# Kernel tuning notes

Hardware: AMD Instinct MI355X
Metric: run time of the kernel (lower is better)

## Reference

```python
import jax, jax.numpy as jnp
import numpy as np

N_HEAD = 12

def setup_inputs() -> dict:
    key = jax.random.key(0)
    ks = jax.random.split(key, 5)
    B, T, C = 4, 2048, 768
    x = jax.random.normal(ks[0], (B, T, C), dtype=jnp.float32)
    s_in = 1.0 / np.sqrt(C)
    W_qkv = jax.random.normal(ks[1], (C, 3 * C), dtype=jnp.float32) * s_in
    b_qkv = jnp.zeros((3 * C,), dtype=jnp.float32)
    W_proj = jax.random.normal(ks[2], (C, C), dtype=jnp.float32) * s_in
    b_proj = jnp.zeros((C,), dtype=jnp.float32)
    return {"x": x, "W_qkv": W_qkv, "b_qkv": b_qkv, "W_proj": W_proj, "b_proj": b_proj}


def reference(x, W_qkv, b_qkv, W_proj, b_proj):
    B, T, C = x.shape
    H = N_HEAD
    D = C // H  # head dim
    qkv = x @ W_qkv + b_qkv                      # [B,T,3C]
    q, k, v = jnp.split(qkv, 3, axis=-1)
    # [B,T,C] -> [B,H,T,D]
    q = q.reshape(B, T, H, D).transpose(0, 2, 1, 3)
    k = k.reshape(B, T, H, D).transpose(0, 2, 1, 3)
    v = v.reshape(B, T, H, D).transpose(0, 2, 1, 3)
    att = jnp.einsum("bhqd,bhkd->bhqk", q, k) / jnp.sqrt(jnp.asarray(D, x.dtype))
    causal = jnp.tril(jnp.ones((T, T), dtype=bool))
    att = jnp.where(causal, att, jnp.asarray(-jnp.inf, att.dtype))
    att = jax.nn.softmax(att, axis=-1)
    y = jnp.einsum("bhqk,bhkd->bhqd", att, v)    # [B,H,T,D]
    y = y.transpose(0, 2, 1, 3).reshape(B, T, C)
    return y @ W_proj + b_proj
```

## Files before the change

### kernel.cpp

```cpp
#include <hip/hip_runtime.h>
#include <hip/hip_bf16.h>

typedef __bf16 bf16x8 __attribute__((ext_vector_type(8)));
typedef float f32x4 __attribute__((ext_vector_type(4)));
typedef unsigned int u32x4 __attribute__((ext_vector_type(4)));
typedef unsigned int u32x2 __attribute__((ext_vector_type(2)));
typedef int i32x2 __attribute__((ext_vector_type(2)));
typedef unsigned short u16;
typedef unsigned long long u64;

#define WAITVM(n) asm volatile("s_waitcnt vmcnt(" #n ")" ::: "memory")
#define SBAR() asm volatile("s_barrier" ::: "memory")

__device__ __forceinline__ u16 f2bf(float f) {
  unsigned u = __builtin_bit_cast(unsigned, f);
  u += 0x7FFFu + ((u >> 16) & 1u);
  return (u16)(u >> 16);
}
__device__ __forceinline__ unsigned cvtpk(float a, float b) {
  float2 f; f.x = a; f.y = b;
  __hip_bfloat162 h = __float22bfloat162_rn(f);
  unsigned u;
  __builtin_memcpy(&u, &h, 4);
  return u;
}

__device__ __forceinline__ void plswap(unsigned &a, unsigned &b) {
  i32x2 r = __builtin_amdgcn_permlane32_swap((int)a, (int)b, false, false);
  a = (unsigned)r[0];
  b = (unsigned)r[1];
}

__device__ __forceinline__ void gll16(const u16* g, u16* l) {
  __builtin_amdgcn_global_load_lds(
      (const __attribute__((address_space(1))) unsigned int*)g,
      (__attribute__((address_space(3))) unsigned int*)l, 16, 0, 0);
}

__global__ void cast_x_kernel(const float* __restrict__ in, u16* __restrict__ out, int n4) {
  int i = blockIdx.x * blockDim.x + threadIdx.x;
  if (i >= n4) return;
  f32x4 v = *(const f32x4*)(in + (size_t)i * 4);
  u32x2 pk;
  pk[0] = cvtpk(v[0], v[1]);
  pk[1] = cvtpk(v[2], v[3]);
  *(u32x2*)(out + (size_t)i * 4) = pk;
}

__global__ void transpose_cast_kernel(const float* __restrict__ W, u16* __restrict__ WT, int K, int N) {
  __shared__ float tile[32][33];
  int c0 = blockIdx.x * 32, r0 = blockIdx.y * 32;
  int tx = threadIdx.x & 31, tg = threadIdx.x >> 5;
#pragma unroll
  for (int i = 0; i < 4; ++i) {
    int r = tg + i * 8;
    tile[r][tx] = W[(size_t)(r0 + r) * N + c0 + tx];
  }
  __syncthreads();
#pragma unroll
  for (int i = 0; i < 4; ++i) {
    int r = tg + i * 8;
    WT[(size_t)(c0 + r) * K + r0 + tx] = f2bf(tile[tx][r]);
  }
}

__global__ __launch_bounds__(256, 4) void gemm_qkv_kernel(
    const u16* __restrict__ A, const u16* __restrict__ BT, const float* __restrict__ bias,
    u16* __restrict__ Qb, u16* __restrict__ Kb, u16* __restrict__ Vt) {
  constexpr int K = 768;
  constexpr int NS = K / 32;
  __shared__ u16 Asm[2][128 * 32];
  __shared__ u16 Bsm[2][128 * 32];
  const int lin = blockIdx.y * 18 + blockIdx.x;
  const int swz = (lin & 7) * 144 + (lin >> 3);
  const int bxn = swz % 18, byn = swz / 18;
  const int tid = threadIdx.x;
  const int w = tid >> 6, lane = tid & 63;
  const int l15 = lane & 15, quad = lane >> 4;
  const int srow = tid >> 2, scol = (tid & 3) * 8;
  const int m0 = byn * 128, n0 = bxn * 128;
  const u16* Ag = A + (size_t)(m0 + srow) * K + scol;
  const u16* Bg = BT + (size_t)(n0 + srow) * K + scol;
  const int mw = (w >> 1) * 64, nw = (w & 1) * 64;
  f32x4 acc[4][4];
#pragma unroll
  for (int i = 0; i < 4; ++i)
#pragma unroll
    for (int j = 0; j < 4; ++j) acc[i][j] = {0.f, 0.f, 0.f, 0.f};

  auto STAGE = [&](int buf, int ks) {
    const u16* a = Ag + ks * 32;
    const u16* b = Bg + ks * 32;
#pragma unroll
    for (int rb = 0; rb < 2; ++rb) {
      gll16(a + (size_t)rb * 64 * K, &Asm[buf][(rb * 64 + w * 16) * 32]);
      gll16(b + (size_t)rb * 64 * K, &Bsm[buf][(rb * 64 + w * 16) * 32]);
    }
  };
  auto COMPUTE = [&](int buf) {
    bf16x8 af[4], bfj[4];
#pragma unroll
    for (int i = 0; i < 4; ++i) af[i] = *(const bf16x8*)&Asm[buf][(mw + i * 16 + l15) * 32 + quad * 8];
#pragma unroll
    for (int j = 0; j < 4; ++j) bfj[j] = *(const bf16x8*)&Bsm[buf][(nw + j * 16 + l15) * 32 + quad * 8];
#pragma unroll
    for (int i = 0; i < 4; ++i)
#pragma unroll
      for (int j = 0; j < 4; ++j)
        acc[i][j] = __builtin_amdgcn_mfma_f32_16x16x32_bf16(af[i], bfj[j], acc[i][j], 0, 0, 0);
  };

  STAGE(0, 0);
  for (int s = 0; s + 2 < NS; s += 2) {
    STAGE(1, s + 1); WAITVM(4); SBAR(); COMPUTE(0); SBAR();
    STAGE(0, s + 2); WAITVM(4); SBAR(); COMPUTE(1); SBAR();
  }
  STAGE(1, NS - 1); WAITVM(4); SBAR(); COMPUTE(0);
  WAITVM(0); SBAR(); COMPUTE(1);

  const int sec = bxn / 6;
  const int nbase = n0 - sec * 768;
#pragma unroll
  for (int j = 0; j < 4; ++j) {
    const int nloc = nbase + nw + j * 16 + l15;
    const float bv = bias[sec * 768 + nloc];
    const int h = nloc >> 6, d = nloc & 63;
#pragma unroll
    for (int i = 0; i < 4; ++i) {
      const int m = m0 + mw + i * 16 + quad * 4;
      const int bb = m >> 11, trow = m & 2047;
      if (sec == 2) {
        u32x2 pk;
        pk[0] = cvtpk(acc[i][j][0] + bv, acc[i][j][1] + bv);
        pk[1] = cvtpk(acc[i][j][2] + bv, acc[i][j][3] + bv);
        *(u32x2*)(Vt + (size_t)((bb * 12 + h) * 64 + d) * 2048 + trow) = pk;
      } else {
        u16* dst = (sec == 0) ? Qb : Kb;
        const float scl = (sec == 0) ? 0.125f * 1.44269504f : 1.0f;
#pragma unroll
        for (int r = 0; r < 4; ++r)
          dst[(size_t)((bb * 12 + h) * 2048 + trow + r) * 64 + d] = f2bf((acc[i][j][r] + bv) * scl);
      }
    }
  }
}

__global__ __launch_bounds__(256, 4) void gemm_proj_kernel(
    const u16* __restrict__ A, const u16* __restrict__ BT, const float* __restrict__ bias,
    float* __restrict__ out) {
  constexpr int K = 768;
  constexpr int NS = K / 32;
  __shared__ u16 Asm[2][64 * 32];
  __shared__ u16 Bsm[2][128 * 32];
  const int lin = blockIdx.y * 6 + blockIdx.x;
  const int swz = (lin & 7) * 96 + (lin >> 3);
  const int tid = threadIdx.x;
  const int w = tid >> 6, lane = tid & 63;
  const int l15 = lane & 15, quad = lane >> 4;
  const int srow = tid >> 2, scol = (tid & 3) * 8;
  const int m0 = (swz / 6) * 64, n0 = (swz % 6) * 128;
  const u16* Ag = A + (size_t)(m0 + srow) * K + scol;
  const u16* Bg = BT + (size_t)(n0 + srow) * K + scol;
  const int mw = (w >> 1) * 32, nw = (w & 1) * 64;
  f32x4 acc[2][4];
#pragma unroll
  for (int i = 0; i < 2; ++i)
#pragma unroll
    for (int j = 0; j < 4; ++j) acc[i][j] = {0.f, 0.f, 0.f, 0.f};

  auto STAGE = [&](int buf, int ks) {
    const u16* a = Ag + ks * 32;
    const u16* b = Bg + ks * 32;
    gll16(a, &Asm[buf][(w * 16) * 32]);
#pragma unroll
    for (int rb = 0; rb < 2; ++rb)
      gll16(b + (size_t)rb * 64 * K, &Bsm[buf][(rb * 64 + w * 16) * 32]);
  };
  auto COMPUTE = [&](int buf) {
    bf16x8 af[2], bfj[4];
#pragma unroll
    for (int i = 0; i < 2; ++i) af[i] = *(const bf16x8*)&Asm[buf][(mw + i * 16 + l15) * 32 + quad * 8];
#pragma unroll
    for (int j = 0; j < 4; ++j) bfj[j] = *(const bf16x8*)&Bsm[buf][(nw + j * 16 + l15) * 32 + quad * 8];
#pragma unroll
    for (int i = 0; i < 2; ++i)
#pragma unroll
      for (int j = 0; j < 4; ++j)
        acc[i][j] = __builtin_amdgcn_mfma_f32_16x16x32_bf16(af[i], bfj[j], acc[i][j], 0, 0, 0);
  };

  STAGE(0, 0);
  for (int s = 0; s + 2 < NS; s += 2) {
    STAGE(1, s + 1); WAITVM(3); SBAR(); COMPUTE(0); SBAR();
    STAGE(0, s + 2); WAITVM(3); SBAR(); COMPUTE(1); SBAR();
  }
  STAGE(1, NS - 1); WAITVM(3); SBAR(); COMPUTE(0);
  WAITVM(0); SBAR(); COMPUTE(1);

#pragma unroll
  for (int j = 0; j < 4; ++j) {
    const int n = n0 + nw + j * 16 + l15;
    const float bv = bias[n];
#pragma unroll
    for (int i = 0; i < 2; ++i) {
      const int m = m0 + mw + i * 16 + quad * 4;
#pragma unroll
      for (int r = 0; r < 4; ++r) out[(size_t)(m + r) * 768 + n] = acc[i][j][r] + bv;
    }
  }
}

__global__ __launch_bounds__(512) void attn_split_kernel(
    const u16* __restrict__ Qg, const u16* __restrict__ Kg, const u16* __restrict__ Vtg,
    u16* __restrict__ Yb, float* __restrict__ Opart, float* __restrict__ lpart) {
  constexpr int T = 2048, D = 64;
  constexpr int LDP = 72;
  constexpr float MBOUND = 20.0f;
  __shared__ u16 Ks[2][64 * LDP];
  __shared__ u16 VTs[2][64 * LDP];
  const int lin = blockIdx.y * 40 + blockIdx.x;
  const int swzb = (lin & 7) * 240 + (lin >> 3);
  const int s = 39 - (swzb % 40);
  const int bh = swzb / 40;
  int qt2, c;
  if (s < 4) { qt2 = s; c = 0; }
  else if (s < 12) { qt2 = 4 + ((s - 4) >> 1); c = (s - 4) & 1; }
  else if (s < 24) { int u = s - 12; int q3 = u / 3; qt2 = 8 + q3; c = u - 3 * q3; }
  else { int u = s - 24; qt2 = 12 + (u >> 2); c = u & 3; }
  const int nkt = 2 * qt2 + 2;
  const int niter = min(8, nkt - 8 * c);
  const int tid = threadIdx.x;
  const int w = tid >> 6, lane = tid & 63;
  const int l15 = lane & 15, quad = lane >> 4;
  const int srow = tid >> 3;
  const int scol = (tid & 7) * 8;
  const int so0 = scol - 4 * (tid & 1);
  const int so1 = scol + 8 - 4 * (tid & 1);
  const u16* Kp = Kg + (size_t)bh * T * D;
  const u16* VTp = Vtg + (size_t)bh * D * T;

  const int wdiag = 2 * qt2 + (w >> 2);
  const int qq = qt2 * 128 + w * 16 + l15;
  const u16* qrow = Qg + ((size_t)bh * T + qq) * D;
  const bf16x8 qfa = *(const bf16x8*)(qrow + quad * 8);
  const bf16x8 qfb = *(const bf16x8*)(qrow + 32 + quad * 8);

  u32x4 onesw; onesw[0] = 0x3F803F80u; onesw[1] = 0x3F803F80u; onesw[2] = 0x3F803F80u; onesw[3] = 0x3F803F80u;
  const bf16x8 ones = __builtin_bit_cast(bf16x8, onesw);

  f32x4 o[4] = {{0,0,0,0},{0,0,0,0},{0,0,0,0},{0,0,0,0}};
  f32x4 lacc = {0.f, 0.f, 0.f, 0.f};

  u32x4 kA, vA;
  auto LOADT = [&](int kt) {
    const int k1 = kt * 64;
    kA = *(const u32x4*)(Kp + (size_t)(k1 + srow) * D + scol);
    vA = *(const u32x4*)(VTp + (size_t)srow * T + k1 + scol);
  };
  auto STORET = [&](int buf) {
    *(u32x4*)&Ks[buf][srow * LDP + scol] = kA;
    u32x2 vlo; vlo[0] = vA[0]; vlo[1] = vA[1];
    u32x2 vhi; vhi[0] = vA[2]; vhi[1] = vA[3];
    *(u32x2*)&VTs[buf][srow * LDP + so0] = vlo;
    *(u32x2*)&VTs[buf][srow * LDP + so1] = vhi;
  };

  LOADT(c * 8);
  STORET(0);
  if (niter > 1) LOADT(c * 8 + 1);
  __syncthreads();

  for (int j = 0; j < niter; ++j) {
    const int buf = j & 1;
    const int ktg = c * 8 + j;
    if (ktg <= wdiag) {
      f32x4 sA[4];
#pragma unroll
      for (int t = 0; t < 4; ++t) sA[t] = {-MBOUND, -MBOUND, -MBOUND, -MBOUND};
      __builtin_amdgcn_s_setprio(1);
#pragma unroll
      for (int t = 0; t < 4; ++t) {
        const bf16x8 kf0 = *(const bf16x8*)&Ks[buf][(t * 16 + l15) * LDP + quad * 8];
        const bf16x8 kf1 = *(const bf16x8*)&Ks[buf][(t * 16 + l15) * LDP + 32 + quad * 8];
        sA[t] = __builtin_amdgcn_mfma_f32_16x16x32_bf16(kf0, qfa, sA[t], 0, 0, 0);
        sA[t] = __builtin_amdgcn_mfma_f32_16x16x32_bf16(kf1, qfb, sA[t], 0, 0, 0);
      }
      __builtin_amdgcn_s_setprio(0);
      if (ktg == wdiag) {
        const int k0 = ktg * 64;
#pragma unroll
        for (int t = 0; t < 4; ++t)
#pragma unroll
          for (int r = 0; r < 4; ++r)
            if (k0 + t * 16 + quad * 4 + r > qq) sA[t][r] = -1e30f;
      }
      unsigned W[4][2];
#pragma unroll
      for (int t = 0; t < 4; ++t) {
        float e0 = __builtin_amdgcn_exp2f(sA[t][0]);
        float e1 = __builtin_amdgcn_exp2f(sA[t][1]);
        float e2 = __builtin_amdgcn_exp2f(sA[t][2]);
        float e3 = __builtin_amdgcn_exp2f(sA[t][3]);
        W[t][0] = cvtpk(e0, e1);
        W[t][1] = cvtpk(e2, e3);
      }
      plswap(W[0][0], W[1][0]);
      plswap(W[0][1], W[1][1]);
      plswap(W[2][0], W[3][0]);
      plswap(W[2][1], W[3][1]);
      u32x4 paw; paw[0] = W[0][0]; paw[1] = W[0][1]; paw[2] = W[1][0]; paw[3] = W[1][1];
      u32x4 pbw; pbw[0] = W[2][0]; pbw[1] = W[2][1]; pbw[2] = W[3][0]; pbw[3] = W[3][1];
      const bf16x8 pa = __builtin_bit_cast(bf16x8, paw);
      const bf16x8 pb = __builtin_bit_cast(bf16x8, pbw);
      __builtin_amdgcn_s_setprio(1);
      lacc = __builtin_amdgcn_mfma_f32_16x16x32_bf16(ones, pa, lacc, 0, 0, 0);
      lacc = __builtin_amdgcn_mfma_f32_16x16x32_bf16(ones, pb, lacc, 0, 0, 0);
#pragma unroll
      for (int t = 0; t < 4; ++t) {
        const bf16x8 vf0 = *(const bf16x8*)&VTs[buf][(t * 16 + l15) * LDP + quad * 8];
        const bf16x8 vf1 = *(const bf16x8*)&VTs[buf][(t * 16 + l15) * LDP + 32 + quad * 8];
        o[t] = __builtin_amdgcn_mfma_f32_16x16x32_bf16(vf0, pa, o[t], 0, 0, 0);
        o[t] = __builtin_amdgcn_mfma_f32_16x16x32_bf16(vf1, pb, o[t], 0, 0, 0);
      }
      __builtin_amdgcn_s_setprio(0);
    }
    if (j + 1 < niter) {
      STORET(buf ^ 1);
      if (j + 2 < niter) LOADT(c * 8 + j + 2);
    }
    __syncthreads();
  }

  const float lv = lacc[0];
  if (qt2 <= 3) {
    const float inv = 1.f / lv;
    const int bidx = bh / 12, hidx = bh % 12;
    u16* y = Yb + ((size_t)bidx * T + qq) * 768 + hidx * 64;
#pragma unroll
    for (int t = 0; t < 4; ++t) {
      u32x2 pk;
      pk[0] = cvtpk(o[t][0] * inv, o[t][1] * inv);
      pk[1] = cvtpk(o[t][2] * inv, o[t][3] * inv);
      *(u32x2*)(y + t * 16 + quad * 4) = pk;
    }
  } else {
    const size_t pidx = (size_t)bh * 40 + s;
    float* Op = Opart + pidx * 8192 + (size_t)(w * 16 + l15) * 64;
#pragma unroll
    for (int t = 0; t < 4; ++t) *(f32x4*)(Op + t * 16 + quad * 4) = o[t];
    if (quad == 0) lpart[pidx * 128 + w * 16 + l15] = lv;
  }
}

__global__ __launch_bounds__(256) void attn_combine_kernel(
    const float* __restrict__ Opart, const float* __restrict__ lpart, u16* __restrict__ Yb) {
  constexpr int T = 2048;
  const int qt2 = 4 + blockIdx.x;
  const int bh = blockIdx.y;
  const int nch = (qt2 < 8) ? 2 : (qt2 < 12) ? 3 : 4;
  const int off = (qt2 < 8) ? 4 + (qt2 - 4) * 2 : (qt2 < 12) ? 12 + (qt2 - 8) * 3 : 24 + (qt2 - 12) * 4;
  const size_t base = (size_t)bh * 40 + off;
  const int tid = threadIdx.x;
  const int q = tid >> 1, db = (tid & 1) * 32;
  f32x4 o[8] = {{0,0,0,0},{0,0,0,0},{0,0,0,0},{0,0,0,0},{0,0,0,0},{0,0,0,0},{0,0,0,0},{0,0,0,0}};
  float l = 0.f;
  for (int cc = 0; cc < nch; ++cc) {
    const float* Op = Opart + (base + cc) * 8192 + (size_t)q * 64 + db;
#pragma unroll
    for (int v = 0; v < 8; ++v) o[v] += *(const f32x4*)(Op + v * 4);
    l += lpart[(base + cc) * 128 + q];
  }
  const float inv = 1.f / l;
  const int bidx = bh / 12, hidx = bh % 12;
  u16* y = Yb + ((size_t)bidx * T + qt2 * 128 + q) * 768 + hidx * 64 + db;
#pragma unroll
  for (int g = 0; g < 2; ++g) {
    u32x4 pk;
    pk[0] = cvtpk(o[g * 4 + 0][0] * inv, o[g * 4 + 0][1] * inv);
    pk[1] = cvtpk(o[g * 4 + 0][2] * inv, o[g * 4 + 0][3] * inv);
    pk[2] = cvtpk(o[g * 4 + 1][0] * inv, o[g * 4 + 1][1] * inv);
    pk[3] = cvtpk(o[g * 4 + 1][2] * inv, o[g * 4 + 1][3] * inv);
    *(u32x4*)(y + g * 16) = pk;
    pk[0] = cvtpk(o[g * 4 + 2][0] * inv, o[g * 4 + 2][1] * inv);
    pk[1] = cvtpk(o[g * 4 + 2][2] * inv, o[g * 4 + 2][3] * inv);
    pk[2] = cvtpk(o[g * 4 + 3][0] * inv, o[g * 4 + 3][1] * inv);
    pk[3] = cvtpk(o[g * 4 + 3][2] * inv, o[g * 4 + 3][3] * inv);
    *(u32x4*)(y + g * 16 + 8) = pk;
  }
}

__global__ __launch_bounds__(256) void attn_kernel(
    const u16* __restrict__ Qg, const u16* __restrict__ Kg, const u16* __restrict__ Vtg,
    u16* __restrict__ Yb) {
  constexpr int T = 2048, D = 64;
  constexpr int LDP = 72;
  constexpr float MBOUND = 20.0f;
  __shared__ u16 Ks[64 * LDP];
  __shared__ u16 VTs[64 * LDP];
  __shared__ u16 Ps[4 * 32 * LDP];
  const int qb = 15 - blockIdx.x;
  const int bh = blockIdx.y;
  const int Q0 = qb * 128;
  const int bidx = bh / 12, hidx = bh % 12;
  const int tid = threadIdx.x;
  const int w = tid >> 6, lane = tid & 63;
  const int l15 = lane & 15, quad = lane >> 4;
  const int srow = tid >> 2, scol = (tid & 3) * 16;
  const u16* Kp = Kg + (size_t)bh * T * D;
  const u16* VTp = Vtg + (size_t)bh * D * T;
  u16* pw0 = &Ps[(w * 32) * LDP];
  u16* pw1 = &Ps[(w * 32 + 16) * LDP];
  const u16* qrow0 = Qg + ((size_t)bh * T + Q0 + w * 16 + l15) * D;
  const bf16x8 qf0a = *(const bf16x8*)(qrow0 + quad * 8);
  const bf16x8 qf0b = *(const bf16x8*)(qrow0 + 32 + quad * 8);
  const bf16x8 qf1a = *(const bf16x8*)(qrow0 + (size_t)64 * D + quad * 8);
  const bf16x8 qf1b = *(const bf16x8*)(qrow0 + (size_t)64 * D + 32 + quad * 8);
  const int qq0 = Q0 + w * 16 + l15, qq1 = qq0 + 64;
  f32x4 o0[4] = {{0,0,0,0},{0,0,0,0},{0,0,0,0},{0,0,0,0}};
  f32x4 o1[4] = {{0,0,0,0},{0,0,0,0},{0,0,0,0},{0,0,0,0}};
  float l0v = 0.f, l1v = 0.f;
  const int nkt = 2 * qb + 2;
  u32x4 kA = *(const u32x4*)(Kp + (size_t)srow * D + scol);
  u32x4 kB = *(const u32x4*)(Kp + (size_t)srow * D + scol + 8);
  u32x4 vA = *(const u32x4*)(VTp + (size_t)srow * T + scol);
  u32x4 vB = *(const u32x4*)(VTp + (size_t)srow * T + scol + 8);
  for (int kt = 0; kt < nkt; ++kt) {
    __syncthreads();
    *(u32x4*)&Ks[srow * LDP + scol] = kA;
    *(u32x4*)&Ks[srow * LDP + scol + 8] = kB;
    *(u32x4*)&VTs[srow * LDP + scol] = vA;
    *(u32x4*)&VTs[srow * LDP + scol + 8] = vB;
    __syncthreads();
    if (kt + 1 < nkt) {
      const int k1 = (kt + 1) * 64;
      kA = *(const u32x4*)(Kp + (size_t)(k1 + srow) * D + scol);
      kB = *(const u32x4*)(Kp + (size_t)(k1 + srow) * D + scol + 8);
      vA = *(const u32x4*)(VTp + (size_t)srow * T + k1 + scol);
      vB = *(const u32x4*)(VTp + (size_t)srow * T + k1 + scol + 8);
    }
    const int k0 = kt * 64;
    const bool g0a = (kt <= 2 * qb);
    f32x4 s0[4] = {{0,0,0,0},{0,0,0,0},{0,0,0,0},{0,0,0,0}};
    f32x4 s1[4] = {{0,0,0,0},{0,0,0,0},{0,0,0,0},{0,0,0,0}};
#pragma unroll
    for (int t = 0; t < 4; ++t) {
      const bf16x8 kf0 = *(const bf16x8*)&Ks[(t * 16 + l15) * LDP + quad * 8];
      const bf16x8 kf1 = *(const bf16x8*)&Ks[(t * 16 + l15) * LDP + 32 + quad * 8];
      s0[t] = __builtin_amdgcn_mfma_f32_16x16x32_bf16(kf0, qf0a, s0[t], 0, 0, 0);
      s0[t] = __builtin_amdgcn_mfma_f32_16x16x32_bf16(kf1, qf0b, s0[t], 0, 0, 0);
      s1[t] = __builtin_amdgcn_mfma_f32_16x16x32_bf16(kf0, qf1a, s1[t], 0, 0, 0);
      s1[t] = __builtin_amdgcn_mfma_f32_16x16x32_bf16(kf1, qf1b, s1[t], 0, 0, 0);
    }
    if (g0a) {
      if (kt == 2 * qb) {
#pragma unroll
        for (int t = 0; t < 4; ++t)
#pragma unroll
          for (int r = 0; r < 4; ++r)
            if (k0 + t * 16 + quad * 4 + r > qq0) s0[t][r] = -1e30f;
      }
#pragma unroll
      for (int t = 0; t < 4; ++t) {
        float e0 = __builtin_amdgcn_exp2f(s0[t][0] - MBOUND);
        float e1 = __builtin_amdgcn_exp2f(s0[t][1] - MBOUND);
        float e2 = __builtin_amdgcn_exp2f(s0[t][2] - MBOUND);
        float e3 = __builtin_amdgcn_exp2f(s0[t][3] - MBOUND);
        l0v += (e0 + e1) + (e2 + e3);
        u32x2 pk;
        pk[0] = cvtpk(e0, e1);
        pk[1] = cvtpk(e2, e3);
        *(u32x2*)&pw0[l15 * LDP + t * 16 + quad * 4] = pk;
      }
    }
    {
      if (kt == 2 * qb + 1) {
#pragma unroll
        for (int t = 0; t < 4; ++t)
#pragma unroll
          for (int r = 0; r < 4; ++r)
            if (k0 + t * 16 + quad * 4 + r > qq1) s1[t][r] = -1e30f;
      }
#pragma unroll
      for (int t = 0; t < 4; ++t) {
        float e0 = __builtin_amdgcn_exp2f(s1[t][0] - MBOUND);
        float e1 = __builtin_amdgcn_exp2f(s1[t][1] - MBOUND);
        float e2 = __builtin_amdgcn_exp2f(s1[t][2] - MBOUND);
        float e3 = __builtin_amdgcn_exp2f(s1[t][3] - MBOUND);
        l1v += (e0 + e1) + (e2 + e3);
        u32x2 pk;
        pk[0] = cvtpk(e0, e1);
        pk[1] = cvtpk(e2, e3);
        *(u32x2*)&pw1[l15 * LDP + t * 16 + quad * 4] = pk;
      }
    }
    const bf16x8 p0a = *(const bf16x8*)&pw0[l15 * LDP + quad * 8];
    const bf16x8 p0b = *(const bf16x8*)&pw0[l15 * LDP + 32 + quad * 8];
    const bf16x8 p1a = *(const bf16x8*)&pw1[l15 * LDP + quad * 8];
    const bf16x8 p1b = *(const bf16x8*)&pw1[l15 * LDP + 32 + quad * 8];
#pragma unroll
    for (int t = 0; t < 4; ++t) {
      const bf16x8 vf0 = *(const bf16x8*)&VTs[(t * 16 + l15) * LDP + quad * 8];
      const bf16x8 vf1 = *(const bf16x8*)&VTs[(t * 16 + l15) * LDP + 32 + quad * 8];
      if (g0a) {
        o0[t] = __builtin_amdgcn_mfma_f32_16x16x32_bf16(vf0, p0a, o0[t], 0, 0, 0);
        o0[t] = __builtin_amdgcn_mfma_f32_16x16x32_bf16(vf1, p0b, o0[t], 0, 0, 0);
      }
      o1[t] = __builtin_amdgcn_mfma_f32_16x16x32_bf16(vf0, p1a, o1[t], 0, 0, 0);
      o1[t] = __builtin_amdgcn_mfma_f32_16x16x32_bf16(vf1, p1b, o1[t], 0, 0, 0);
    }
  }
  l0v += __shfl_xor(l0v, 16); l0v += __shfl_xor(l0v, 32);
  l1v += __shfl_xor(l1v, 16); l1v += __shfl_xor(l1v, 32);
  const float inv0 = 1.f / l0v, inv1 = 1.f / l1v;
  u16* y0 = Yb + ((size_t)bidx * T + qq0) * 768 + hidx * 64;
  u16* y1 = Yb + ((size_t)bidx * T + qq1) * 768 + hidx * 64;
#pragma unroll
  for (int t = 0; t < 4; ++t) {
    u32x2 pk0, pk1;
    pk0[0] = cvtpk(o0[t][0] * inv0, o0[t][1] * inv0);
    pk0[1] = cvtpk(o0[t][2] * inv0, o0[t][3] * inv0);
    pk1[0] = cvtpk(o1[t][0] * inv1, o1[t][1] * inv1);
    pk1[1] = cvtpk(o1[t][2] * inv1, o1[t][3] * inv1);
    *(u32x2*)(y0 + t * 16 + quad * 4) = pk0;
    *(u32x2*)(y1 + t * 16 + quad * 4) = pk1;
  }
}

extern "C" void kernel_launch(void* const* d_in, const int* in_sizes, int n_in,
                              void* d_out, int out_size, void* d_ws, size_t ws_size,
                              hipStream_t stream) {
  const float* x = (const float*)d_in[0];
  const float* W_qkv = (const float*)d_in[1];
  const float* b_qkv = (const float*)d_in[2];
  const float* W_proj = (const float*)d_in[3];
  const float* b_proj = (const float*)d_in[4];
  float* out = (float*)d_out;

  constexpr size_t MC = (size_t)8192 * 768;
  u16* xb = (u16*)d_ws;
  u16* Qb = xb + MC;
  u16* Kb = Qb + MC;
  u16* Vt = Kb + MC;
  u16* Yb = Vt + MC;
  u16* WqkvT = Yb + MC;
  u16* WprojT = WqkvT + (size_t)2304 * 768;
  constexpr size_t BASE_U16 = 5 * MC + (size_t)2304 * 768 + (size_t)768 * 768;
  float* Opart = (float*)((u16*)d_ws + BASE_U16);
  float* lpart = Opart + (size_t)1920 * 8192;
  constexpr size_t NEED = BASE_U16 * 2 + ((size_t)1920 * 8192 + (size_t)1920 * 128) * 4;
  const bool use_split = (ws_size >= NEED);

  cast_x_kernel<<<6291456 / (4 * 256), 256, 0, stream>>>(x, xb, 6291456 / 4);
  transpose_cast_kernel<<<dim3(2304 / 32, 768 / 32), 256, 0, stream>>>(W_qkv, WqkvT, 768, 2304);
  transpose_cast_kernel<<<dim3(768 / 32, 768 / 32), 256, 0, stream>>>(W_proj, WprojT, 768, 768);
  gemm_qkv_kernel<<<dim3(18, 64), 256, 0, stream>>>(xb, WqkvT, b_qkv, Qb, Kb, Vt);
  if (use_split) {
    attn_split_kernel<<<dim3(40, 48), 512, 0, stream>>>(Qb, Kb, Vt, Yb, Opart, lpart);
    attn_combine_kernel<<<dim3(12, 48), 256, 0, stream>>>(Opart, lpart, Yb);
  } else {
    attn_kernel<<<dim3(16, 48), 256, 0, stream>>>(Qb, Kb, Vt, Yb);
  }
  gemm_proj_kernel<<<dim3(6, 128), 256, 0, stream>>>(Yb, WprojT, b_proj, out);
}
```

Baseline: 226.5 us.

## Fuse fp32-to-bf16 cast of x into QKV GEMM A-tile loading

Removes the separate cast_x kernel. The QKV GEMM now loads fp32 x directly into registers, converts it to bf16 and writes it to LDS, while B still uses direct global-to-LDS loads. The GEMM also drops the block-index swizzle, and both GEMM pipelines move to a single-step loop that waits on all loads plus a barrier every k-step. This saves one launch and the 8192x768 bf16 round trip through memory, but doubles A-operand global traffic inside the GEMM and serialises the pipeline more, which can expose load latency.

```diff
diff --git a/kernel.cpp b/kernel.cpp
--- a/kernel.cpp
+++ b/kernel.cpp
@@ -10,6 +10,7 @@
 typedef unsigned long long u64;
 
 #define WAITVM(n) asm volatile("s_waitcnt vmcnt(" #n ")" ::: "memory")
+#define WAITLG() asm volatile("s_waitcnt lgkmcnt(0)" ::: "memory")
 #define SBAR() asm volatile("s_barrier" ::: "memory")
 
 __device__ __forceinline__ u16 f2bf(float f) {
@@ -37,16 +38,6 @@
       (__attribute__((address_space(3))) unsigned int*)l, 16, 0, 0);
 }
 
-__global__ void cast_x_kernel(const float* __restrict__ in, u16* __restrict__ out, int n4) {
-  int i = blockIdx.x * blockDim.x + threadIdx.x;
-  if (i >= n4) return;
-  f32x4 v = *(const f32x4*)(in + (size_t)i * 4);
-  u32x2 pk;
-  pk[0] = cvtpk(v[0], v[1]);
-  pk[1] = cvtpk(v[2], v[3]);
-  *(u32x2*)(out + (size_t)i * 4) = pk;
-}
-
 __global__ void transpose_cast_kernel(const float* __restrict__ W, u16* __restrict__ WT, int K, int N) {
   __shared__ float tile[32][33];
   int c0 = blockIdx.x * 32, r0 = blockIdx.y * 32;
@@ -65,21 +56,19 @@
 }
 
 __global__ __launch_bounds__(256, 4) void gemm_qkv_kernel(
-    const u16* __restrict__ A, const u16* __restrict__ BT, const float* __restrict__ bias,
+    const float* __restrict__ X, const u16* __restrict__ BT, const float* __restrict__ bias,
     u16* __restrict__ Qb, u16* __restrict__ Kb, u16* __restrict__ Vt) {
   constexpr int K = 768;
   constexpr int NS = K / 32;
   __shared__ u16 Asm[2][128 * 32];
   __shared__ u16 Bsm[2][128 * 32];
-  const int lin = blockIdx.y * 18 + blockIdx.x;
-  const int swz = (lin & 7) * 144 + (lin >> 3);
-  const int bxn = swz % 18, byn = swz / 18;
   const int tid = threadIdx.x;
   const int w = tid >> 6, lane = tid & 63;
   const int l15 = lane & 15, quad = lane >> 4;
   const int srow = tid >> 2, scol = (tid & 3) * 8;
-  const int m0 = byn * 128, n0 = bxn * 128;
-  const u16* Ag = A + (size_t)(m0 + srow) * K + scol;
+  const int m0 = blockIdx.y * 128, n0 = blockIdx.x * 128;
+  const float* Xg0 = X + (size_t)(m0 + srow) * K + scol;
+  const float* Xg1 = X + (size_t)(m0 + 64 + srow) * K + scol;
   const u16* Bg = BT + (size_t)(n0 + srow) * K + scol;
   const int mw = (w >> 1) * 64, nw = (w & 1) * 64;
   f32x4 acc[4][4];
@@ -88,14 +77,26 @@
 #pragma unroll
     for (int j = 0; j < 4; ++j) acc[i][j] = {0.f, 0.f, 0.f, 0.f};
 
-  auto STAGE = [&](int buf, int ks) {
-    const u16* a = Ag + ks * 32;
+  f32x4 a0l, a0h, a1l, a1h;
+  auto LOADA = [&](int ks) {
+    const float* p0 = Xg0 + ks * 32;
+    const float* p1 = Xg1 + ks * 32;
+    a0l = *(const f32x4*)p0; a0h = *(const f32x4*)(p0 + 4);
+    a1l = *(const f32x4*)p1; a1h = *(const f32x4*)(p1 + 4);
+  };
+  auto WRITEA = [&](int buf) {
+    u32x4 p0, p1;
+    p0[0] = cvtpk(a0l[0], a0l[1]); p0[1] = cvtpk(a0l[2], a0l[3]);
+    p0[2] = cvtpk(a0h[0], a0h[1]); p0[3] = cvtpk(a0h[2], a0h[3]);
+    p1[0] = cvtpk(a1l[0], a1l[1]); p1[1] = cvtpk(a1l[2], a1l[3]);
+    p1[2] = cvtpk(a1h[0], a1h[1]); p1[3] = cvtpk(a1h[2], a1h[3]);
+    *(u32x4*)&Asm[buf][srow * 32 + scol] = p0;
+    *(u32x4*)&Asm[buf][(64 + srow) * 32 + scol] = p1;
+  };
+  auto STAGEB = [&](int buf, int ks) {
     const u16* b = Bg + ks * 32;
-#pragma unroll
-    for (int rb = 0; rb < 2; ++rb) {
-      gll16(a + (size_t)rb * 64 * K, &Asm[buf][(rb * 64 + w * 16) * 32]);
-      gll16(b + (size_t)rb * 64 * K, &Bsm[buf][(rb * 64 + w * 16) * 32]);
-    }
+    gll16(b, &Bsm[buf][(w * 16) * 32]);
+    gll16(b + (size_t)64 * K, &Bsm[buf][(64 + w * 16) * 32]);
   };
   auto COMPUTE = [&](int buf) {
     bf16x8 af[4], bfj[4];
@@ -110,15 +111,19 @@
         acc[i][j] = __builtin_amdgcn_mfma_f32_16x16x32_bf16(af[i], bfj[j], acc[i][j], 0, 0, 0);
   };
 
-  STAGE(0, 0);
-  for (int s = 0; s + 2 < NS; s += 2) {
-    STAGE(1, s + 1); WAITVM(4); SBAR(); COMPUTE(0); SBAR();
-    STAGE(0, s + 2); WAITVM(4); SBAR(); COMPUTE(1); SBAR();
-  }
-  STAGE(1, NS - 1); WAITVM(4); SBAR(); COMPUTE(0);
-  WAITVM(0); SBAR(); COMPUTE(1);
-
-  const int sec = bxn / 6;
+  LOADA(0);
+  STAGEB(0, 0);
+  WRITEA(0);
+  WAITVM(0); WAITLG(); SBAR();
+  for (int s = 0; s < NS; ++s) {
+    const int buf = s & 1;
+    if (s + 1 < NS) { LOADA(s + 1); STAGEB(buf ^ 1, s + 1); }
+    COMPUTE(buf);
+    if (s + 1 < NS) WRITEA(buf ^ 1);
+    WAITVM(0); WAITLG(); SBAR();
+  }
+
+  const int sec = blockIdx.x / 6;
   const int nbase = n0 - sec * 768;
 #pragma unroll
   for (int j = 0; j < 4; ++j) {
@@ -190,12 +195,13 @@
   };
 
   STAGE(0, 0);
-  for (int s = 0; s + 2 < NS; s += 2) {
-    STAGE(1, s + 1); WAITVM(3); SBAR(); COMPUTE(0); SBAR();
-    STAGE(0, s + 2); WAITVM(3); SBAR(); COMPUTE(1); SBAR();
-  }
-  STAGE(1, NS - 1); WAITVM(3); SBAR(); COMPUTE(0);
-  WAITVM(0); SBAR(); COMPUTE(1);
+  WAITVM(0); SBAR();
+  for (int s = 0; s < NS; ++s) {
+    const int buf = s & 1;
+    if (s + 1 < NS) STAGE(buf ^ 1, s + 1);
+    COMPUTE(buf);
+    WAITVM(0); SBAR();
+  }
 
 #pragma unroll
   for (int j = 0; j < 4; ++j) {
@@ -550,10 +556,9 @@
   constexpr size_t NEED = BASE_U16 * 2 + ((size_t)1920 * 8192 + (size_t)1920 * 128) * 4;
   const bool use_split = (ws_size >= NEED);
 
-  cast_x_kernel<<<6291456 / (4 * 256), 256, 0, stream>>>(x, xb, 6291456 / 4);
   transpose_cast_kernel<<<dim3(2304 / 32, 768 / 32), 256, 0, stream>>>(W_qkv, WqkvT, 768, 2304);
   transpose_cast_kernel<<<dim3(768 / 32, 768 / 32), 256, 0, stream>>>(W_proj, WprojT, 768, 768);
-  gemm_qkv_kernel<<<dim3(18, 64), 256, 0, stream>>>(xb, WqkvT, b_qkv, Qb, Kb, Vt);
+  gemm_qkv_kernel<<<dim3(18, 64), 256, 0, stream>>>(x, WqkvT, b_qkv, Qb, Kb, Vt);
   if (use_split) {
     attn_split_kernel<<<dim3(40, 48), 512, 0, stream>>>(Qb, Kb, Vt, Yb, Opart, lpart);
     attn_combine_kernel<<<dim3(12, 48), 256, 0, stream>>>(Opart, lpart, Yb);
```

Result: slower. 250.1 us (+10.4%).

## Enlarge QKV GEMM tile to 256x128 with 512 threads, simplify proj pipeline

Applied to the files above, without the earlier changes.

The QKV GEMM now uses 512-thread blocks covering 256 rows by 128 columns, so each B tile loaded from global memory is reused across twice as many rows. The grid halves in the M dimension and the block-index swizzle is removed. The projection GEMM's double-buffered loop is rewritten as a single loop that issues the next stage, computes, then waits on all loads with a barrier. That wait-all pattern may expose more load latency than the previous partial vmcnt scheme, and dropping the swizzle may reduce L2 locality.

```diff
diff --git a/kernel.cpp b/kernel.cpp
--- a/kernel.cpp
+++ b/kernel.cpp
@@ -64,23 +64,20 @@
   }
 }
 
-__global__ __launch_bounds__(256, 4) void gemm_qkv_kernel(
+__global__ __launch_bounds__(512) void gemm_qkv_kernel(
     const u16* __restrict__ A, const u16* __restrict__ BT, const float* __restrict__ bias,
     u16* __restrict__ Qb, u16* __restrict__ Kb, u16* __restrict__ Vt) {
   constexpr int K = 768;
   constexpr int NS = K / 32;
-  __shared__ u16 Asm[2][128 * 32];
+  __shared__ u16 Asm[2][256 * 32];
   __shared__ u16 Bsm[2][128 * 32];
-  const int lin = blockIdx.y * 18 + blockIdx.x;
-  const int swz = (lin & 7) * 144 + (lin >> 3);
-  const int bxn = swz % 18, byn = swz / 18;
   const int tid = threadIdx.x;
   const int w = tid >> 6, lane = tid & 63;
   const int l15 = lane & 15, quad = lane >> 4;
   const int srow = tid >> 2, scol = (tid & 3) * 8;
-  const int m0 = byn * 128, n0 = bxn * 128;
+  const int m0 = blockIdx.y * 256, n0 = blockIdx.x * 128;
   const u16* Ag = A + (size_t)(m0 + srow) * K + scol;
-  const u16* Bg = BT + (size_t)(n0 + srow) * K + scol;
+  const u16* Bg = BT + (size_t)(n0 + (srow & 127)) * K + scol;
   const int mw = (w >> 1) * 64, nw = (w & 1) * 64;
   f32x4 acc[4][4];
 #pragma unroll
@@ -90,12 +87,9 @@
 
   auto STAGE = [&](int buf, int ks) {
     const u16* a = Ag + ks * 32;
-    const u16* b = Bg + ks * 32;
-#pragma unroll
-    for (int rb = 0; rb < 2; ++rb) {
-      gll16(a + (size_t)rb * 64 * K, &Asm[buf][(rb * 64 + w * 16) * 32]);
-      gll16(b + (size_t)rb * 64 * K, &Bsm[buf][(rb * 64 + w * 16) * 32]);
-    }
+    gll16(a, &Asm[buf][(w * 16) * 32]);
+    gll16(a + (size_t)128 * K, &Asm[buf][(128 + w * 16) * 32]);
+    gll16(Bg + ks * 32, &Bsm[buf][(w * 16) * 32]);
   };
   auto COMPUTE = [&](int buf) {
     bf16x8 af[4], bfj[4];
@@ -112,13 +106,13 @@
 
   STAGE(0, 0);
   for (int s = 0; s + 2 < NS; s += 2) {
-    STAGE(1, s + 1); WAITVM(4); SBAR(); COMPUTE(0); SBAR();
-    STAGE(0, s + 2); WAITVM(4); SBAR(); COMPUTE(1); SBAR();
-  }
-  STAGE(1, NS - 1); WAITVM(4); SBAR(); COMPUTE(0);
+    STAGE(1, s + 1); WAITVM(3); SBAR(); COMPUTE(0); SBAR();
+    STAGE(0, s + 2); WAITVM(3); SBAR(); COMPUTE(1); SBAR();
+  }
+  STAGE(1, NS - 1); WAITVM(3); SBAR(); COMPUTE(0);
   WAITVM(0); SBAR(); COMPUTE(1);
 
-  const int sec = bxn / 6;
+  const int sec = blockIdx.x / 6;
   const int nbase = n0 - sec * 768;
 #pragma unroll
   for (int j = 0; j < 4; ++j) {
@@ -190,12 +184,13 @@
   };
 
   STAGE(0, 0);
-  for (int s = 0; s + 2 < NS; s += 2) {
-    STAGE(1, s + 1); WAITVM(3); SBAR(); COMPUTE(0); SBAR();
-    STAGE(0, s + 2); WAITVM(3); SBAR(); COMPUTE(1); SBAR();
-  }
-  STAGE(1, NS - 1); WAITVM(3); SBAR(); COMPUTE(0);
-  WAITVM(0); SBAR(); COMPUTE(1);
+  WAITVM(0); SBAR();
+  for (int s = 0; s < NS; ++s) {
+    const int buf = s & 1;
+    if (s + 1 < NS) STAGE(buf ^ 1, s + 1);
+    COMPUTE(buf);
+    WAITVM(0); SBAR();
+  }
 
 #pragma unroll
   for (int j = 0; j < 4; ++j) {
@@ -553,7 +548,7 @@
   cast_x_kernel<<<6291456 / (4 * 256), 256, 0, stream>>>(x, xb, 6291456 / 4);
   transpose_cast_kernel<<<dim3(2304 / 32, 768 / 32), 256, 0, stream>>>(W_qkv, WqkvT, 768, 2304);
   transpose_cast_kernel<<<dim3(768 / 32, 768 / 32), 256, 0, stream>>>(W_proj, WprojT, 768, 768);
-  gemm_qkv_kernel<<<dim3(18, 64), 256, 0, stream>>>(xb, WqkvT, b_qkv, Qb, Kb, Vt);
+  gemm_qkv_kernel<<<dim3(18, 32), 512, 0, stream>>>(xb, WqkvT, b_qkv, Qb, Kb, Vt);
   if (use_split) {
     attn_split_kernel<<<dim3(40, 48), 512, 0, stream>>>(Qb, Kb, Vt, Yb, Opart, lpart);
     attn_combine_kernel<<<dim3(12, 48), 256, 0, stream>>>(Opart, lpart, Yb);
```

New measurement: 239.9 us. 5.9% more time.
